# Performance work log

Measured on AMD Instinct MI355X. Metric: run time of the kernel, lower is better.

The kernel has to match this reference:

```python
import jax, jax.numpy as jnp
import numpy as np

IN_DIM = 512
REDUCED = IN_DIM // 8  # reduction_ratio = 8
B, C, H, W = 8, 32, 64, IN_DIM


def setup_inputs() -> dict:
    key = jax.random.key(0)
    ks = jax.random.split(key, 9)
    s_in = 1.0 / np.sqrt(IN_DIM)
    inp = {
        "x": jax.random.normal(ks[0], (B, C, H, W), dtype=jnp.float32),
        # torch Linear weights stored here as [in, out] for y = x @ w + b
        "wq": jax.random.uniform(ks[1], (IN_DIM, REDUCED), jnp.float32, -s_in, s_in),
        "bq": jax.random.uniform(ks[2], (REDUCED,), jnp.float32, -s_in, s_in),
        "wk": jax.random.uniform(ks[3], (IN_DIM, REDUCED), jnp.float32, -s_in, s_in),
        "bk": jax.random.uniform(ks[4], (REDUCED,), jnp.float32, -s_in, s_in),
        "wv": jax.random.uniform(ks[5], (IN_DIM, IN_DIM), jnp.float32, -s_in, s_in),
        "bv": jax.random.uniform(ks[6], (IN_DIM,), jnp.float32, -s_in, s_in),
        "wo": jax.random.uniform(ks[7], (IN_DIM, IN_DIM), jnp.float32, -s_in, s_in),
        "bo": jax.random.uniform(ks[8], (IN_DIM,), jnp.float32, -s_in, s_in),
    }
    return inp


def reference(x, wq, bq, wk, bk, wv, bv, wo, bo):
    b, c, h, w = x.shape
    n = c * h  # attention tokens = flattened C*H positions, feature dim = W
    q = (x @ wq + bq).reshape(b, n, REDUCED)   # [B, N, r]
    k = (x @ wk + bk).reshape(b, n, REDUCED)   # [B, N, r]
    v = (x @ wv + bv).reshape(b, n, w)         # [B, N, W]
    energy = jnp.einsum("bnr,bmr->bnm", q, k)  # [B, N, N]
    attn = jax.nn.softmax(energy, axis=-1)
    out = jnp.einsum("bnm,bmd->bnd", attn, v).reshape(b, c, h, w)
    out = out @ wo + bo
    return out + x
```

## Files before the change

### kernel.cpp

```cpp
#include <hip/hip_runtime.h>

typedef __bf16 bf16x8 __attribute__((ext_vector_type(8)));
typedef float  f32x4  __attribute__((ext_vector_type(4)));

union U8 { uint4 v; unsigned short u[8]; };

static __device__ __forceinline__ float bf2f(unsigned short u) {
    union { unsigned int i; float f; } c; c.i = ((unsigned int)u) << 16; return c.f;
}
static __device__ __forceinline__ unsigned short f2bf(float f) {
    union { float f; unsigned int i; } c; c.f = f;
    unsigned int x = c.i;
    unsigned int r = (x + 0x7FFFu + ((x >> 16) & 1u)) >> 16;
    return (unsigned short)r;
}

static __device__ __forceinline__ U8 load8(const float* p) {
    U8 r;
    const float4 a = *(const float4*)p;
    const float4 b = *(const float4*)(p + 4);
    r.u[0] = f2bf(a.x); r.u[1] = f2bf(a.y); r.u[2] = f2bf(a.z); r.u[3] = f2bf(a.w);
    r.u[4] = f2bf(b.x); r.u[5] = f2bf(b.y); r.u[6] = f2bf(b.z); r.u[7] = f2bf(b.w);
    return r;
}

static __device__ __forceinline__ void gld_lds16(const void* g, void* l) {
    __builtin_amdgcn_global_load_lds(
        (const __attribute__((address_space(1))) unsigned int*)g,
        (__attribute__((address_space(3))) unsigned int*)l, 16, 0, 0);
}

__global__ __launch_bounds__(256)
void pack(const float* __restrict__ x, unsigned short* __restrict__ xb,
          const float* __restrict__ bq, const float* __restrict__ bk,
          const float* __restrict__ bv, float* __restrict__ ball,
          const float* __restrict__ wv, const float* __restrict__ wo,
          const float* __restrict__ wq, const float* __restrict__ wk,
          unsigned short* __restrict__ wAllT, unsigned short* __restrict__ woT)
{
    const int bid = blockIdx.x, t = threadIdx.x;
    if (bid < 2048) {
        const long i = ((long)bid * 256 + t) * 16;
        U8 a = load8(x + i);
        U8 b = load8(x + i + 8);
        *(uint4*)(xb + i) = a.v;
        *(uint4*)(xb + i + 8) = b.v;
        if (bid == 0) {
            ball[t]       = t < 64 ? bq[t] : (t < 128 ? bk[t - 64] : bv[t - 128]);
            ball[t + 256] = bv[t + 128];
            if (t < 128) ball[t + 512] = bv[t + 384];
        }
        return;
    }
    __shared__ float sT[64][65];
    const int b2 = bid - 2048;
    const int zz = b2 >> 6, rem = b2 & 63;
    const int cx = rem & 7, ry = rem >> 3;
    const float* src; unsigned short* dst; int C;
    if      (zz == 0) { src = wv; dst = wAllT + 128 * 512; C = 512; }
    else if (zz == 1) { src = wo; dst = woT;               C = 512; }
    else if (zz == 2) { src = wq; dst = wAllT;             C = 64;  }
    else              { src = wk; dst = wAllT + 64 * 512;  C = 64;  }
    const int R = 512;
    const int c0 = cx * 64, r0 = ry * 64;
    if (c0 >= C) return;
    #pragma unroll
    for (int k = 0; k < 16; ++k) {
        const int lin = k * 256 + t;
        const int i = lin >> 6, j = lin & 63;
        sT[i][j] = src[(long)(r0 + i) * C + c0 + j];
    }
    __syncthreads();
    #pragma unroll
    for (int k = 0; k < 16; ++k) {
        const int lin = k * 256 + t;
        const int o = lin >> 6, i2 = lin & 63;
        dst[(long)(c0 + o) * R + r0 + i2] = f2bf(sT[i2][o]);
    }
}

template<bool BIAS, bool RES, bool OUT_F32, bool MIXED, int NCOL>
__global__ __launch_bounds__(256, 3)
void gemm64(const unsigned short* __restrict__ A, int lda,
            const unsigned short* __restrict__ B, int ldb,
            void* __restrict__ Cp, int ldc,
            void* __restrict__ Cp2,
            const float* __restrict__ bias,
            const float* __restrict__ resid,
            int K)
{
    __shared__ __align__(16) unsigned short sMem[2][12288];

    const int t = threadIdx.x, wave = t >> 6, lane = t & 63;
    const int lr = lane & 15, quad = lane >> 4;

    const int bid = blockIdx.x;
    const int sw  = (bid & 7) * (NCOL * 32) + (bid >> 3);
    const int rowBase = (sw / NCOL) * 64;
    const int colBase = (sw % NCOL) * 128;
    const int wm = (wave & 1) * 32, wn = (wave >> 1) * 64;

    const int srow  = lane >> 3;
    const int sslot = lane & 7;
    const int swz   = (sslot ^ srow) << 4;

    f32x4 acc[2][4];
    #pragma unroll
    for (int mt = 0; mt < 2; ++mt)
        #pragma unroll
        for (int nt = 0; nt < 4; ++nt) acc[mt][nt] = (f32x4){0.f, 0.f, 0.f, 0.f};

    auto STAGE = [&](int buf, int kt) {
        unsigned short* sA = sMem[buf];
        unsigned short* sB = sMem[buf] + 4096;
        #pragma unroll
        for (int is = 0; is < 2; ++is) {
            const int r0 = wave * 16 + is * 8;
            gld_lds16((const char*)A + ((long)(rowBase + r0 + srow) * lda + kt) * 2 + swz,
                      (char*)sA + r0 * 128);
        }
        #pragma unroll
        for (int is = 0; is < 4; ++is) {
            const int r0 = wave * 32 + is * 8;
            gld_lds16((const char*)B + ((long)(colBase + r0 + srow) * ldb + kt) * 2 + swz,
                      (char*)sB + r0 * 128);
        }
    };

    STAGE(0, 0);
    __syncthreads();

    int cur = 0;
    for (int kt = 0; kt < K; kt += 64) {
        if (kt + 64 < K) STAGE(cur ^ 1, kt + 64);

        const unsigned short* sA = sMem[cur];
        const unsigned short* sB = sMem[cur] + 4096;
        #pragma unroll
        for (int ks = 0; ks < 2; ++ks) {
            const int kb = ks * 64 + quad * 16;
            bf16x8 bfr[4];
            #pragma unroll
            for (int nt = 0; nt < 4; ++nt) {
                const int row = wn + nt * 16 + lr;
                bfr[nt] = *(const bf16x8*)((const char*)sB + row * 128 + (kb ^ ((row & 7) << 4)));
            }
            #pragma unroll
            for (int mt = 0; mt < 2; ++mt) {
                const int row = wm + mt * 16 + lr;
                bf16x8 af = *(const bf16x8*)((const char*)sA + row * 128 + (kb ^ ((row & 7) << 4)));
                #pragma unroll
                for (int nt = 0; nt < 4; ++nt)
                    acc[mt][nt] = __builtin_amdgcn_mfma_f32_16x16x32_bf16(af, bfr[nt], acc[mt][nt], 0, 0, 0);
            }
        }
        __syncthreads();
        cur ^= 1;
    }

    if (MIXED && colBase >= 128) {
        unsigned short* sT = sMem[0];
        #pragma unroll
        for (int mt = 0; mt < 2; ++mt)
            #pragma unroll
            for (int nt = 0; nt < 4; ++nt) {
                const int row0 = wm + mt * 16 + quad * 4;
                const int col  = wn + nt * 16 + lr;
                const float b = BIAS ? bias[colBase + col] : 0.f;
                ushort4 v4;
                v4.x = f2bf(acc[mt][nt][0] + b);
                v4.y = f2bf(acc[mt][nt][1] + b);
                v4.z = f2bf(acc[mt][nt][2] + b);
                v4.w = f2bf(acc[mt][nt][3] + b);
                *(ushort4*)&sT[col * 72 + row0] = v4;
            }
        __syncthreads();
        unsigned short* C2 = (unsigned short*)Cp2;
        const int bat = rowBase >> 11, key0 = rowBase & 2047;
        const long vcol0 = colBase - 128;
        #pragma unroll
        for (int ro = 0; ro < 4; ++ro) {
            const int flat = ro * 256 + t;
            const int col = flat >> 3, ch = flat & 7;
            const uint4 v = *(const uint4*)&sT[col * 72 + ch * 8];
            *(uint4*)&C2[((long)bat * 512 + vcol0 + col) * 2048 + key0 + ch * 8] = v;
        }
        return;
    }

    float* Cf = (float*)Cp;
    unsigned short* Cb = (unsigned short*)Cp;
    #pragma unroll
    for (int mt = 0; mt < 2; ++mt)
        #pragma unroll
        for (int nt = 0; nt < 4; ++nt) {
            const int row0 = rowBase + wm + mt * 16 + quad * 4;
            const int col  = colBase + wn + nt * 16 + lr;
            const float b = BIAS ? bias[col] : 0.f;
            #pragma unroll
            for (int r = 0; r < 4; ++r) {
                const int row = row0 + r;
                float v = acc[mt][nt][r] + b;
                if (RES)     v += resid[(long)row * ldc + col];
                if (OUT_F32) Cf[(long)row * ldc + col] = v;
                else         Cb[(long)row * ldc + col] = f2bf(v);
            }
        }
}

__global__ __launch_bounds__(256, 4)
void flash_attn(const unsigned short* __restrict__ QK,
                const unsigned short* __restrict__ VT,
                unsigned short* __restrict__ O)
{
    __shared__ __align__(16) unsigned short sK[2][64 * 64];
    __shared__ __align__(16) unsigned short sP[2][64 * 72];
    __shared__ float sL[64];

    const int bid = blockIdx.x;
    const int z  = bid & 7;
    const int rr = bid >> 3;
    const int cs = rr & 3;
    const int qt = rr >> 2;

    const int t = threadIdx.x, wave = t >> 6, lane = t & 63;
    const int lr = lane & 15, quad = lane >> 4;

    const long qrow0 = (long)z * 2048 + qt * 64;
    const unsigned short* qp = QK + (qrow0 + wave * 16 + lr) * 128 + quad * 8;
    const bf16x8 qa0 = *(const bf16x8*)(qp);
    const bf16x8 qa1 = *(const bf16x8*)(qp + 32);

    const char* Kb = (const char*)(QK + (long)z * 2048 * 128 + 64);
    const unsigned short* Vb = VT + (long)z * 512 * 2048
                                  + ((long)cs * 128 + wave * 32) * 2048;

    const long stg_go = (long)(wave * 16 + (lane >> 3)) * 256
                      + (((lane & 7) ^ (lane >> 3)) << 4);
    const int swq = (lr & 7) << 4;

    f32x4 acc[4][2];
    #pragma unroll
    for (int mt = 0; mt < 4; ++mt)
        #pragma unroll
        for (int nt = 0; nt < 2; ++nt) acc[mt][nt] = (f32x4){0.f, 0.f, 0.f, 0.f};
    float lsum[4] = {0.f, 0.f, 0.f, 0.f};

    {
        const char* gk = Kb + stg_go;
        char* lk = (char*)sK[0] + wave * 2048;
        gld_lds16(gk, lk);
        gld_lds16(gk + 2048, lk + 1024);
    }
    __syncthreads();

    int cur = 0;
    for (int kt = 0; kt < 32; ++kt) {
        const int key0 = kt * 64;

        bf16x8 vv[2][2];
        #pragma unroll
        for (int nt = 0; nt < 2; ++nt) {
            const unsigned short* vp = Vb + (long)(nt * 16 + lr) * 2048 + key0 + quad * 8;
            vv[nt][0] = *(const bf16x8*)(vp);
            vv[nt][1] = *(const bf16x8*)(vp + 32);
        }

        if (kt < 31) {
            const char* gk = Kb + (long)(kt + 1) * 16384 + stg_go;
            char* lk = (char*)sK[cur ^ 1] + wave * 2048;
            gld_lds16(gk, lk);
            gld_lds16(gk + 2048, lk + 1024);
        }

        const char* sKc = (const char*)sK[cur];
        __bf16* sPb = (__bf16*)sP[cur];
        #pragma unroll
        for (int nt = 0; nt < 4; ++nt) {
            const int kb = (nt * 16 + lr) * 128;
            bf16x8 k0 = *(const bf16x8*)(sKc + kb + ((quad * 16) ^ swq));
            bf16x8 k1 = *(const bf16x8*)(sKc + kb + ((quad * 16 + 64) ^ swq));
            f32x4 sv = (f32x4){0.f, 0.f, 0.f, 0.f};
            sv = __builtin_amdgcn_mfma_f32_16x16x32_bf16(qa0, k0, sv, 0, 0, 0);
            sv = __builtin_amdgcn_mfma_f32_16x16x32_bf16(qa1, k1, sv, 0, 0, 0);
            #pragma unroll
            for (int r = 0; r < 4; ++r) {
                const float e = __expf(sv[r]);
                const __bf16 pb = (__bf16)e;
                lsum[r] += (float)pb;
                sPb[(wave * 16 + quad * 4 + r) * 72 + nt * 16 + lr] = pb;
            }
        }

        __syncthreads();

        const unsigned short* sPc = sP[cur];
        __builtin_amdgcn_s_setprio(1);
        #pragma unroll
        for (int mt = 0; mt < 4; ++mt) {
            const unsigned short* pp = &sPc[(mt * 16 + lr) * 72 + quad * 8];
            bf16x8 p0 = *(const bf16x8*)(pp);
            bf16x8 p1 = *(const bf16x8*)(pp + 32);
            acc[mt][0] = __builtin_amdgcn_mfma_f32_16x16x32_bf16(p0, vv[0][0], acc[mt][0], 0, 0, 0);
            acc[mt][0] = __builtin_amdgcn_mfma_f32_16x16x32_bf16(p1, vv[0][1], acc[mt][0], 0, 0, 0);
            acc[mt][1] = __builtin_amdgcn_mfma_f32_16x16x32_bf16(p0, vv[1][0], acc[mt][1], 0, 0, 0);
            acc[mt][1] = __builtin_amdgcn_mfma_f32_16x16x32_bf16(p1, vv[1][1], acc[mt][1], 0, 0, 0);
        }
        __builtin_amdgcn_s_setprio(0);
        cur ^= 1;
    }

    #pragma unroll
    for (int r = 0; r < 4; ++r) {
        float v = lsum[r];
        v += __shfl_xor(v, 1); v += __shfl_xor(v, 2);
        v += __shfl_xor(v, 4); v += __shfl_xor(v, 8);
        lsum[r] = v;
    }
    if (lr == 0) {
        #pragma unroll
        for (int r = 0; r < 4; ++r) sL[wave * 16 + quad * 4 + r] = lsum[r];
    }
    __syncthreads();

    #pragma unroll
    for (int mt = 0; mt < 4; ++mt) {
        float inv[4];
        #pragma unroll
        for (int r = 0; r < 4; ++r) inv[r] = 1.0f / sL[mt * 16 + quad * 4 + r];
        #pragma unroll
        for (int nt = 0; nt < 2; ++nt) {
            const int col = cs * 128 + wave * 32 + nt * 16 + lr;
            #pragma unroll
            for (int r = 0; r < 4; ++r) {
                const long row = qrow0 + mt * 16 + quad * 4 + r;
                O[row * 512 + col] = f2bf(acc[mt][nt][r] * inv[r]);
            }
        }
    }
}

extern "C" void kernel_launch(void* const* d_in, const int* in_sizes, int n_in,
                              void* d_out, int out_size, void* d_ws, size_t ws_size,
                              hipStream_t stream)
{
    const float* x  = (const float*)d_in[0];
    const float* wq = (const float*)d_in[1];
    const float* bq = (const float*)d_in[2];
    const float* wk = (const float*)d_in[3];
    const float* bk = (const float*)d_in[4];
    const float* wv = (const float*)d_in[5];
    const float* bv = (const float*)d_in[6];
    const float* wo = (const float*)d_in[7];
    const float* bo = (const float*)d_in[8];

    const int W = 512;
    float* out = (float*)d_out;
    dim3 blk(256);
    char* ws = (char*)d_ws;

    const size_t NEED = 56ull << 20;
    if (ws_size < NEED) return;

    unsigned short* QK    = (unsigned short*)(ws);
    unsigned short* VT    = (unsigned short*)(ws + ( 4ull << 20));
    unsigned short* O     = (unsigned short*)(ws + (20ull << 20));
    unsigned short* xb    = (unsigned short*)(ws + (36ull << 20));
    unsigned short* wAllT = (unsigned short*)(ws + (52ull << 20));
    unsigned short* woT   = (unsigned short*)(ws + (53ull << 20));
    float*          ball  = (float*)         (ws + (53ull << 20) + (512ull << 10));

    pack<<<dim3(2048 + 256), blk, 0, stream>>>(x, xb, bq, bk, bv, ball,
                                               wv, wo, wq, wk, wAllT, woT);

    gemm64<true, false, false, true, 5><<<dim3(1280), blk, 0, stream>>>(
        xb, W, wAllT, W, QK, 128, VT, ball, nullptr, W);

    flash_attn<<<dim3(1024), blk, 0, stream>>>(QK, VT, O);

    gemm64<true, true, true, false, 4><<<dim3(1024), blk, 0, stream>>>(
        O, W, woT, W, out, W, nullptr, bo, x, W);
}
```

Before: 212.7 us.

## Warp-specialize flash attention with 512-thread blocks and separate K-load waves

The attention kernel now launches 512-thread blocks, each covering 256 output columns instead of 128, so the grid shrinks from 1024 to 512 blocks. This halves how many times the QK^T scores and exponentials are recomputed across column slices. Waves 0-3 compute scores and probabilities, waves 4-7 only prefetch K tiles into LDS, and all eight waves run the P·V MFMAs. The launch bound of (512, 4) tightens the per-thread register budget, which risks spills, and idle producer or consumer waves could expose latency.

```diff
diff --git a/kernel.cpp b/kernel.cpp
--- a/kernel.cpp
+++ b/kernel.cpp
@@ -208,7 +208,7 @@
         }
 }
 
-__global__ __launch_bounds__(256, 4)
+__global__ __launch_bounds__(512, 4)
 void flash_attn(const unsigned short* __restrict__ QK,
                 const unsigned short* __restrict__ VT,
                 unsigned short* __restrict__ O)
@@ -220,22 +220,27 @@
     const int bid = blockIdx.x;
     const int z  = bid & 7;
     const int rr = bid >> 3;
-    const int cs = rr & 3;
-    const int qt = rr >> 2;
+    const int cs = rr & 1;
+    const int qt = rr >> 1;
 
     const int t = threadIdx.x, wave = t >> 6, lane = t & 63;
     const int lr = lane & 15, quad = lane >> 4;
+    const int sw = wave & 3;
+    const bool isS = wave < 4;
 
     const long qrow0 = (long)z * 2048 + qt * 64;
-    const unsigned short* qp = QK + (qrow0 + wave * 16 + lr) * 128 + quad * 8;
-    const bf16x8 qa0 = *(const bf16x8*)(qp);
-    const bf16x8 qa1 = *(const bf16x8*)(qp + 32);
+    bf16x8 qa0, qa1;
+    if (isS) {
+        const unsigned short* qp = QK + (qrow0 + sw * 16 + lr) * 128 + quad * 8;
+        qa0 = *(const bf16x8*)(qp);
+        qa1 = *(const bf16x8*)(qp + 32);
+    }
 
     const char* Kb = (const char*)(QK + (long)z * 2048 * 128 + 64);
     const unsigned short* Vb = VT + (long)z * 512 * 2048
-                                  + ((long)cs * 128 + wave * 32) * 2048;
-
-    const long stg_go = (long)(wave * 16 + (lane >> 3)) * 256
+                                  + ((long)cs * 256 + wave * 32) * 2048;
+
+    const long stg_go = (long)(sw * 16 + (lane >> 3)) * 256
                       + (((lane & 7) ^ (lane >> 3)) << 4);
     const int swq = (lr & 7) << 4;
 
@@ -246,9 +251,9 @@
         for (int nt = 0; nt < 2; ++nt) acc[mt][nt] = (f32x4){0.f, 0.f, 0.f, 0.f};
     float lsum[4] = {0.f, 0.f, 0.f, 0.f};
 
-    {
+    if (!isS) {
         const char* gk = Kb + stg_go;
-        char* lk = (char*)sK[0] + wave * 2048;
+        char* lk = (char*)sK[0] + sw * 2048;
         gld_lds16(gk, lk);
         gld_lds16(gk + 2048, lk + 1024);
     }
@@ -266,29 +271,31 @@
             vv[nt][1] = *(const bf16x8*)(vp + 32);
         }
 
-        if (kt < 31) {
-            const char* gk = Kb + (long)(kt + 1) * 16384 + stg_go;
-            char* lk = (char*)sK[cur ^ 1] + wave * 2048;
-            gld_lds16(gk, lk);
-            gld_lds16(gk + 2048, lk + 1024);
-        }
-
-        const char* sKc = (const char*)sK[cur];
-        __bf16* sPb = (__bf16*)sP[cur];
-        #pragma unroll
-        for (int nt = 0; nt < 4; ++nt) {
-            const int kb = (nt * 16 + lr) * 128;
-            bf16x8 k0 = *(const bf16x8*)(sKc + kb + ((quad * 16) ^ swq));
-            bf16x8 k1 = *(const bf16x8*)(sKc + kb + ((quad * 16 + 64) ^ swq));
-            f32x4 sv = (f32x4){0.f, 0.f, 0.f, 0.f};
-            sv = __builtin_amdgcn_mfma_f32_16x16x32_bf16(qa0, k0, sv, 0, 0, 0);
-            sv = __builtin_amdgcn_mfma_f32_16x16x32_bf16(qa1, k1, sv, 0, 0, 0);
-            #pragma unroll
-            for (int r = 0; r < 4; ++r) {
-                const float e = __expf(sv[r]);
-                const __bf16 pb = (__bf16)e;
-                lsum[r] += (float)pb;
-                sPb[(wave * 16 + quad * 4 + r) * 72 + nt * 16 + lr] = pb;
+        if (!isS) {
+            if (kt < 31) {
+                const char* gk = Kb + (long)(kt + 1) * 16384 + stg_go;
+                char* lk = (char*)sK[cur ^ 1] + sw * 2048;
+                gld_lds16(gk, lk);
+                gld_lds16(gk + 2048, lk + 1024);
+            }
+        } else {
+            const char* sKc = (const char*)sK[cur];
+            __bf16* sPb = (__bf16*)sP[cur];
+            #pragma unroll
+            for (int nt = 0; nt < 4; ++nt) {
+                const int kb = (nt * 16 + lr) * 128;
+                bf16x8 k0 = *(const bf16x8*)(sKc + kb + ((quad * 16) ^ swq));
+                bf16x8 k1 = *(const bf16x8*)(sKc + kb + ((quad * 16 + 64) ^ swq));
+                f32x4 sv = (f32x4){0.f, 0.f, 0.f, 0.f};
+                sv = __builtin_amdgcn_mfma_f32_16x16x32_bf16(qa0, k0, sv, 0, 0, 0);
+                sv = __builtin_amdgcn_mfma_f32_16x16x32_bf16(qa1, k1, sv, 0, 0, 0);
+                #pragma unroll
+                for (int r = 0; r < 4; ++r) {
+                    const float e = __expf(sv[r]);
+                    const __bf16 pb = (__bf16)e;
+                    lsum[r] += (float)pb;
+                    sPb[(sw * 16 + quad * 4 + r) * 72 + nt * 16 + lr] = pb;
+                }
             }
         }
 
@@ -310,16 +317,18 @@
         cur ^= 1;
     }
 
-    #pragma unroll
-    for (int r = 0; r < 4; ++r) {
-        float v = lsum[r];
-        v += __shfl_xor(v, 1); v += __shfl_xor(v, 2);
-        v += __shfl_xor(v, 4); v += __shfl_xor(v, 8);
-        lsum[r] = v;
-    }
-    if (lr == 0) {
-        #pragma unroll
-        for (int r = 0; r < 4; ++r) sL[wave * 16 + quad * 4 + r] = lsum[r];
+    if (isS) {
+        #pragma unroll
+        for (int r = 0; r < 4; ++r) {
+            float v = lsum[r];
+            v += __shfl_xor(v, 1); v += __shfl_xor(v, 2);
+            v += __shfl_xor(v, 4); v += __shfl_xor(v, 8);
+            lsum[r] = v;
+        }
+        if (lr == 0) {
+            #pragma unroll
+            for (int r = 0; r < 4; ++r) sL[sw * 16 + quad * 4 + r] = lsum[r];
+        }
     }
     __syncthreads();
 
@@ -330,7 +339,7 @@
         for (int r = 0; r < 4; ++r) inv[r] = 1.0f / sL[mt * 16 + quad * 4 + r];
         #pragma unroll
         for (int nt = 0; nt < 2; ++nt) {
-            const int col = cs * 128 + wave * 32 + nt * 16 + lr;
+            const int col = cs * 256 + wave * 32 + nt * 16 + lr;
             #pragma unroll
             for (int r = 0; r < 4; ++r) {
                 const long row = qrow0 + mt * 16 + quad * 4 + r;
@@ -376,7 +385,7 @@
     gemm64<true, false, false, true, 5><<<dim3(1280), blk, 0, stream>>>(
         xb, W, wAllT, W, QK, 128, VT, ball, nullptr, W);
 
-    flash_attn<<<dim3(1024), blk, 0, stream>>>(QK, VT, O);
+    flash_attn<<<dim3(512), dim3(512), 0, stream>>>(QK, VT, O);
 
     gemm64<true, true, true, false, 4><<<dim3(1024), blk, 0, stream>>>(
         O, W, woT, W, out, W, nullptr, bo, x, W);
```

New measurement: 203.8 us (median of 2 runs). -4.2%, faster.

## Keep softmax probabilities in registers and stage V through LDS in attention

Applied to the files above, without the earlier changes.

Restructures the flash attention loop so each wave computes a transposed score tile (K as the A operand). The exponentiated probabilities then land directly in the MFMA A-operand layout and stay in registers instead of going through an LDS P buffer. V is now staged asynchronously into swizzled, double-buffered LDS alongside K, with 32-key tiles over 64 iterations instead of 64-key tiles over 32. Each wave owns 16 query rows across all 128 output columns. This removes the P round-trip through shared memory and the direct per-wave global V loads, but adds one barrier per iteration across twice as many iterations.

```diff
diff --git a/kernel.cpp b/kernel.cpp
--- a/kernel.cpp
+++ b/kernel.cpp
@@ -213,8 +213,8 @@
                 const unsigned short* __restrict__ VT,
                 unsigned short* __restrict__ O)
 {
-    __shared__ __align__(16) unsigned short sK[2][64 * 64];
-    __shared__ __align__(16) unsigned short sP[2][64 * 72];
+    __shared__ __align__(16) unsigned short sK[2][32 * 64];
+    __shared__ __align__(16) unsigned short sV[2][128 * 32];
     __shared__ float sL[64];
 
     const int bid = blockIdx.x;
@@ -223,119 +223,99 @@
     const int cs = rr & 3;
     const int qt = rr >> 2;
 
-    const int t = threadIdx.x, wave = t >> 6, lane = t & 63;
-    const int lr = lane & 15, quad = lane >> 4;
+    const int t = threadIdx.x, w = t >> 6, l = t & 63;
+    const int lr = l & 15, quad = l >> 4;
 
     const long qrow0 = (long)z * 2048 + qt * 64;
-    const unsigned short* qp = QK + (qrow0 + wave * 16 + lr) * 128 + quad * 8;
+    const unsigned short* qp = QK + (qrow0 + w * 16 + lr) * 128 + quad * 8;
     const bf16x8 qa0 = *(const bf16x8*)(qp);
     const bf16x8 qa1 = *(const bf16x8*)(qp + 32);
 
-    const char* Kb = (const char*)(QK + (long)z * 2048 * 128 + 64);
-    const unsigned short* Vb = VT + (long)z * 512 * 2048
-                                  + ((long)cs * 128 + wave * 32) * 2048;
-
-    const long stg_go = (long)(wave * 16 + (lane >> 3)) * 256
-                      + (((lane & 7) ^ (lane >> 3)) << 4);
+    const char* KB = (const char*)QK + (long)z * 2048 * 256 + 128;
+    const char* VB = (const char*)VT + ((long)z * 512 + cs * 128) * 4096;
+
+    const long kstg = (long)(w * 8 + (l >> 3)) * 256 + (((l & 7) ^ (l >> 3)) << 4);
+    const long vstg0 = (long)(w * 32 + (l >> 2)) * 4096 + (((l & 3) ^ ((l >> 3) & 3)) << 4);
+    const long vstg1 = vstg0 + (long)16 * 4096;
+
     const int swq = (lr & 7) << 4;
-
-    f32x4 acc[4][2];
-    #pragma unroll
-    for (int mt = 0; mt < 4; ++mt)
-        #pragma unroll
-        for (int nt = 0; nt < 2; ++nt) acc[mt][nt] = (f32x4){0.f, 0.f, 0.f, 0.f};
-    float lsum[4] = {0.f, 0.f, 0.f, 0.f};
+    const int xv  = (lr >> 1) & 3;
+    const int vb1 = ((((quad >> 1)    ) ^ xv) << 4) + ((quad & 1) << 3);
+    const int vb2 = ((((quad >> 1) + 2) ^ xv) << 4) + ((quad & 1) << 3);
+
+    f32x4 acc[8];
+    #pragma unroll
+    for (int nt = 0; nt < 8; ++nt) acc[nt] = (f32x4){0.f, 0.f, 0.f, 0.f};
+    float lsum = 0.f;
 
     {
-        const char* gk = Kb + stg_go;
-        char* lk = (char*)sK[0] + wave * 2048;
-        gld_lds16(gk, lk);
-        gld_lds16(gk + 2048, lk + 1024);
-    }
-    __syncthreads();
+        gld_lds16(KB + kstg, (char*)sK[0] + w * 1024);
+        gld_lds16(VB + vstg0, (char*)sV[0] + w * 2048);
+        gld_lds16(VB + vstg1, (char*)sV[0] + w * 2048 + 1024);
+    }
 
     int cur = 0;
-    for (int kt = 0; kt < 32; ++kt) {
-        const int key0 = kt * 64;
-
-        bf16x8 vv[2][2];
+    for (int kt = 0; kt < 64; ++kt) {
+        __syncthreads();
+
+        if (kt < 63) {
+            const long kb = (long)(kt + 1) * 8192;
+            const long vb = (long)(kt + 1) * 64;
+            gld_lds16(KB + kb + kstg, (char*)sK[cur ^ 1] + w * 1024);
+            gld_lds16(VB + vb + vstg0, (char*)sV[cur ^ 1] + w * 2048);
+            gld_lds16(VB + vb + vstg1, (char*)sV[cur ^ 1] + w * 2048 + 1024);
+        }
+
+        const char* sKc = (const char*)sK[cur];
+        unsigned int P[4];
         #pragma unroll
         for (int nt = 0; nt < 2; ++nt) {
-            const unsigned short* vp = Vb + (long)(nt * 16 + lr) * 2048 + key0 + quad * 8;
-            vv[nt][0] = *(const bf16x8*)(vp);
-            vv[nt][1] = *(const bf16x8*)(vp + 32);
-        }
-
-        if (kt < 31) {
-            const char* gk = Kb + (long)(kt + 1) * 16384 + stg_go;
-            char* lk = (char*)sK[cur ^ 1] + wave * 2048;
-            gld_lds16(gk, lk);
-            gld_lds16(gk + 2048, lk + 1024);
-        }
-
-        const char* sKc = (const char*)sK[cur];
-        __bf16* sPb = (__bf16*)sP[cur];
-        #pragma unroll
-        for (int nt = 0; nt < 4; ++nt) {
             const int kb = (nt * 16 + lr) * 128;
             bf16x8 k0 = *(const bf16x8*)(sKc + kb + ((quad * 16) ^ swq));
             bf16x8 k1 = *(const bf16x8*)(sKc + kb + ((quad * 16 + 64) ^ swq));
             f32x4 sv = (f32x4){0.f, 0.f, 0.f, 0.f};
-            sv = __builtin_amdgcn_mfma_f32_16x16x32_bf16(qa0, k0, sv, 0, 0, 0);
-            sv = __builtin_amdgcn_mfma_f32_16x16x32_bf16(qa1, k1, sv, 0, 0, 0);
-            #pragma unroll
-            for (int r = 0; r < 4; ++r) {
-                const float e = __expf(sv[r]);
-                const __bf16 pb = (__bf16)e;
-                lsum[r] += (float)pb;
-                sPb[(wave * 16 + quad * 4 + r) * 72 + nt * 16 + lr] = pb;
-            }
-        }
-
-        __syncthreads();
-
-        const unsigned short* sPc = sP[cur];
+            sv = __builtin_amdgcn_mfma_f32_16x16x32_bf16(k0, qa0, sv, 0, 0, 0);
+            sv = __builtin_amdgcn_mfma_f32_16x16x32_bf16(k1, qa1, sv, 0, 0, 0);
+            const unsigned short b0 = f2bf(__expf(sv[0]));
+            const unsigned short b1 = f2bf(__expf(sv[1]));
+            const unsigned short b2 = f2bf(__expf(sv[2]));
+            const unsigned short b3 = f2bf(__expf(sv[3]));
+            lsum += bf2f(b0) + bf2f(b1) + bf2f(b2) + bf2f(b3);
+            P[nt * 2]     = (unsigned int)b0 | ((unsigned int)b1 << 16);
+            P[nt * 2 + 1] = (unsigned int)b2 | ((unsigned int)b3 << 16);
+        }
+        union { unsigned int u[4]; bf16x8 v; } pa;
+        pa.u[0] = P[0]; pa.u[1] = P[1]; pa.u[2] = P[2]; pa.u[3] = P[3];
+
+        const char* sVc = (const char*)sV[cur];
         __builtin_amdgcn_s_setprio(1);
         #pragma unroll
-        for (int mt = 0; mt < 4; ++mt) {
-            const unsigned short* pp = &sPc[(mt * 16 + lr) * 72 + quad * 8];
-            bf16x8 p0 = *(const bf16x8*)(pp);
-            bf16x8 p1 = *(const bf16x8*)(pp + 32);
-            acc[mt][0] = __builtin_amdgcn_mfma_f32_16x16x32_bf16(p0, vv[0][0], acc[mt][0], 0, 0, 0);
-            acc[mt][0] = __builtin_amdgcn_mfma_f32_16x16x32_bf16(p1, vv[0][1], acc[mt][0], 0, 0, 0);
-            acc[mt][1] = __builtin_amdgcn_mfma_f32_16x16x32_bf16(p0, vv[1][0], acc[mt][1], 0, 0, 0);
-            acc[mt][1] = __builtin_amdgcn_mfma_f32_16x16x32_bf16(p1, vv[1][1], acc[mt][1], 0, 0, 0);
+        for (int nt = 0; nt < 8; ++nt) {
+            const int crb = (nt * 16 + lr) * 64;
+            union { unsigned long long u[2]; bf16x8 v; } vf;
+            vf.u[0] = *(const unsigned long long*)(sVc + crb + vb1);
+            vf.u[1] = *(const unsigned long long*)(sVc + crb + vb2);
+            acc[nt] = __builtin_amdgcn_mfma_f32_16x16x32_bf16(pa.v, vf.v, acc[nt], 0, 0, 0);
         }
         __builtin_amdgcn_s_setprio(0);
         cur ^= 1;
     }
 
-    #pragma unroll
-    for (int r = 0; r < 4; ++r) {
-        float v = lsum[r];
-        v += __shfl_xor(v, 1); v += __shfl_xor(v, 2);
-        v += __shfl_xor(v, 4); v += __shfl_xor(v, 8);
-        lsum[r] = v;
-    }
-    if (lr == 0) {
-        #pragma unroll
-        for (int r = 0; r < 4; ++r) sL[wave * 16 + quad * 4 + r] = lsum[r];
-    }
+    lsum += __shfl_xor(lsum, 16);
+    lsum += __shfl_xor(lsum, 32);
+    if (l < 16) sL[w * 16 + l] = lsum;
     __syncthreads();
 
-    #pragma unroll
-    for (int mt = 0; mt < 4; ++mt) {
-        float inv[4];
-        #pragma unroll
-        for (int r = 0; r < 4; ++r) inv[r] = 1.0f / sL[mt * 16 + quad * 4 + r];
-        #pragma unroll
-        for (int nt = 0; nt < 2; ++nt) {
-            const int col = cs * 128 + wave * 32 + nt * 16 + lr;
-            #pragma unroll
-            for (int r = 0; r < 4; ++r) {
-                const long row = qrow0 + mt * 16 + quad * 4 + r;
-                O[row * 512 + col] = f2bf(acc[mt][nt][r] * inv[r]);
-            }
+    float inv[4];
+    #pragma unroll
+    for (int r = 0; r < 4; ++r) inv[r] = 1.0f / sL[w * 16 + quad * 4 + r];
+    #pragma unroll
+    for (int nt = 0; nt < 8; ++nt) {
+        const int col = cs * 128 + nt * 16 + lr;
+        #pragma unroll
+        for (int r = 0; r < 4; ++r) {
+            const long row = qrow0 + w * 16 + quad * 4 + r;
+            O[row * 512 + col] = f2bf(acc[nt][r] * inv[r]);
         }
     }
 }
```

New measurement: 222.2 us. +4.5%, slower.
